# Kernel tuning notes

Measured on AMD Instinct MI355X. Metric: run time of the kernel, lower is better.

The kernel has to match this reference:

```python
import jax, jax.numpy as jnp
import numpy as np
from jax import lax

B = 8192          # batched independent VAD frames (original module is batch=1 streaming)
CUTOFF = 129      # STFT_CUTOFF
STRIDE = 128      # STFT_STRIDE
NFFT = 256        # STFT kernel length (inferred: pad 576->640, stride 128 -> 4 frames)
H = 128           # LSTM hidden size


def conv1d(x, w, b=None, stride=1, padding=0):
    # x: [B, Cin, T], w: [Cout, Cin, K]
    y = lax.conv_general_dilated(x, w, (stride,), [(padding, padding)],
                                 dimension_numbers=("NCH", "OIH", "NCH"))
    if b is not None:
        y = y + b[None, :, None]
    return y


def setup_inputs() -> dict:
    key = jax.random.key(0)
    ks = jax.random.split(key, 40)
    f32 = jnp.float32

    def rn(i, shape, scale=0.1):
        return jax.random.normal(ks[i], shape, dtype=f32) * scale

    inp = {
        "audio": jax.random.normal(ks[0], (B, 576), dtype=f32),
        "h": jnp.zeros((B, H), dtype=f32),
        "c": jnp.zeros((B, H), dtype=f32),
        # STFT basis: 129 real + 129 imag cosine/sine rows, kernel 256
        "forward_basis": rn(1, (2 * CUTOFF, 1, NFFT), 0.1),
        # encoder: 4 conv1d+relu blocks (Silero v5 layout)
        "enc_w1": rn(2, (128, 129, 3)), "enc_b1": rn(3, (128,)),
        "enc_w2": rn(4, (64, 128, 3)), "enc_b2": rn(5, (64,)),
        "enc_w3": rn(6, (64, 64, 3)),  "enc_b3": rn(7, (64,)),
        "enc_w4": rn(8, (128, 64, 3)), "enc_b4": rn(9, (128,)),
        # LSTM cell weights
        "wi": rn(10, (H, H)), "wf": rn(11, (H, H)), "wg": rn(12, (H, H)), "wo": rn(13, (H, H)),
        "ui": rn(14, (H, H)), "uf": rn(15, (H, H)), "ug": rn(16, (H, H)), "uo": rn(17, (H, H)),
        "bxi": rn(18, (H,)), "bxf": rn(19, (H,)), "bxg": rn(20, (H,)), "bxo": rn(21, (H,)),
        "bhi": rn(22, (H,)), "bhf": rn(23, (H,)), "bhg": rn(24, (H,)), "bho": rn(25, (H,)),
        # output head: conv1d 128 -> 1, kernel 1
        "conv_w": rn(26, (1, H, 1)), "conv_b": rn(27, (1,)),
    }
    return inp


def reference(audio, h, c, forward_basis,
              enc_w1, enc_b1, enc_w2, enc_b2, enc_w3, enc_b3, enc_w4, enc_b4,
              wi, wf, wg, wo, ui, uf, ug, uo,
              bxi, bxf, bxg, bxo, bhi, bhf, bhg, bho,
              conv_w, conv_b):
    # STFT via strided conv1d on reflect-padded audio
    x = jnp.pad(audio, ((0, 0), (0, 64)), mode="reflect")[:, None, :]   # [B,1,640]
    x = conv1d(x, forward_basis, stride=STRIDE)                          # [B,258,4]
    real, imag = x[:, :CUTOFF, :], x[:, CUTOFF:, :]
    mag = jnp.sqrt(real ** 2 + imag ** 2)                                # [B,129,4]

    # encoder: conv+relu stack, T: 4 -> 4 -> 2 -> 1 -> 1
    e = jax.nn.relu(conv1d(mag, enc_w1, enc_b1, stride=1, padding=1))
    e = jax.nn.relu(conv1d(e, enc_w2, enc_b2, stride=2, padding=1))
    e = jax.nn.relu(conv1d(e, enc_w3, enc_b3, stride=2, padding=1))
    e = jax.nn.relu(conv1d(e, enc_w4, enc_b4, stride=1, padding=1))
    x = e[:, :, 0]                                                       # [B,128]

    lin = lambda v, W, b: v @ W.T + b
    i_gate = jax.nn.sigmoid(lin(x, wi, bxi) + lin(h, ui, bhi))
    f_gate = jax.nn.sigmoid(lin(x, wf, bxf) + lin(h, uf, bhf))
    g_gate = jnp.tanh(lin(x, wg, bxg) + lin(h, ug, bhg))
    o_gate = jax.nn.sigmoid(lin(x, wo, bxo) + lin(h, uo, bho))
    c_out = f_gate * c + i_gate * g_gate
    h_out = o_gate * jnp.tanh(c_out)

    # output head: relu -> conv1d(128->1, k=1) -> sigmoid -> mean over T(=1)
    y = jax.nn.relu(h_out)                                               # [B,128]
    logit = y @ conv_w[0, :, 0] + conv_b[0]                              # [B]
    prob = jax.nn.sigmoid(logit)[:, None]                                # [B,1]
    return prob, h_out, c_out
```

## Files before the change

### kernel.cpp

```cpp
#include <hip/hip_runtime.h>
#include <math.h>

#define BATCH 8192
typedef unsigned short u16;
typedef unsigned int u32;
typedef _Float16 f16;
typedef __attribute__((ext_vector_type(8))) _Float16 f16x8;
typedef __attribute__((ext_vector_type(4))) float f32x4;
typedef __attribute__((ext_vector_type(4))) unsigned short u16x4;

__device__ __forceinline__ float sigm(float v) { return 1.0f / (1.0f + __expf(-v)); }
__device__ __forceinline__ u16 f2h(float f) {
    union { f16 h; u16 u; } v; v.h = (f16)f;
    return v.u;
}
__device__ __forceinline__ f16x8 ffrag(const u16* Bf, int nt, int ch, int nch, int lane) {
    return *(const f16x8*)(Bf + (((size_t)nt * nch + ch) * 64 + lane) * 8);
}
#define MFMA16(a, b, c) __builtin_amdgcn_mfma_f32_16x16x32_f16(a, b, c, 0, 0, 0)

#define S_FBT 69632
#define S_B1  61440
#define S_B2A 16384
#define S_B2B 24576
#define S_B3  8192
#define S_B4  8192
#define S_BL  131072
#define P_FBT 0
#define P_B1  69632
#define P_B2A 131072
#define P_B2B 147456
#define P_B3  172032
#define P_B4  180224
#define P_BL  188416
#define N_PREP 319488

__global__ __launch_bounds__(256) void k_prep(const float* __restrict__ fb,
                                              const float* __restrict__ w1, const float* __restrict__ w2,
                                              const float* __restrict__ w3, const float* __restrict__ w4,
                                              const float* __restrict__ wi, const float* __restrict__ wf,
                                              const float* __restrict__ wg, const float* __restrict__ wo,
                                              const float* __restrict__ ui, const float* __restrict__ uf,
                                              const float* __restrict__ ug, const float* __restrict__ uo,
                                              u16* __restrict__ wsu) {
    const float* Ws[8] = {wi, wf, wg, wo, ui, uf, ug, uo};
    for (int i = blockIdx.x * 256 + threadIdx.x; i < N_PREP; i += gridDim.x * 256) {
        int r = i;
        float v; int P, idx;
        if (r < S_FBT) {
            int f = r >> 9, lane = (r & 511) >> 3, e = r & 7;
            int n = (f >> 3) * 16 + (lane & 15), k = (f & 7) * 32 + (lane >> 4) * 8 + e;
            int c = n >> 1, part = n & 1;
            v = (n < 258) ? fb[(size_t)(c + part * 129) * 256 + k] : 0.f;
            P = P_FBT; idx = r;
        } else if ((r -= S_FBT) < S_B1) {
            int kk = r / 20480, r2 = r - kk * 20480;
            int f = r2 >> 9, lane = (r2 & 511) >> 3, e = r2 & 7;
            int n = (f / 5) * 16 + (lane & 15), k = (f % 5) * 32 + (lane >> 4) * 8 + e;
            v = (k < 129) ? w1[(size_t)n * 387 + k * 3 + kk] : 0.f;
            P = P_B1; idx = r;
        } else if ((r -= S_B1) < S_B2A) {
            int f = r >> 9, lane = (r & 511) >> 3, e = r & 7;
            int n = (f >> 3) * 16 + (lane & 15), k = (f & 7) * 32 + (lane >> 4) * 8 + e;
            v = w2[(size_t)n * 384 + (k & 127) * 3 + (k >> 7) + 1];
            P = P_B2A; idx = r;
        } else if ((r -= S_B2A) < S_B2B) {
            int f = r >> 9, lane = (r & 511) >> 3, e = r & 7;
            int n = (f / 12) * 16 + (lane & 15), k = (f % 12) * 32 + (lane >> 4) * 8 + e;
            v = w2[(size_t)n * 384 + (k & 127) * 3 + (k >> 7)];
            P = P_B2B; idx = r;
        } else if ((r -= S_B2B) < S_B3) {
            int f = r >> 9, lane = (r & 511) >> 3, e = r & 7;
            int n = (f >> 2) * 16 + (lane & 15), k = (f & 3) * 32 + (lane >> 4) * 8 + e;
            v = w3[(size_t)n * 192 + (k & 63) * 3 + (k >> 6) + 1];
            P = P_B3; idx = r;
        } else if ((r -= S_B3) < S_B4) {
            int f = r >> 9, lane = (r & 511) >> 3, e = r & 7;
            int n = (f >> 1) * 16 + (lane & 15), k = (f & 1) * 32 + (lane >> 4) * 8 + e;
            v = w4[(size_t)n * 192 + k * 3 + 1];
            P = P_B4; idx = r;
        } else {
            r -= S_B4;
            int f = r >> 9, lane = (r & 511) >> 3, e = r & 7;
            int n = (f >> 3) * 16 + (lane & 15), k = (f & 7) * 32 + (lane >> 4) * 8 + e;
            int g = n >> 7, j = n & 127;
            v = Ws[g + ((k >= 128) ? 4 : 0)][(size_t)j * 128 + (k & 127)];
            P = P_BL; idx = r;
        }
        wsu[P + idx] = f2h(v);
    }
}

__global__ __launch_bounds__(512, 4) void k_all(const float* __restrict__ audio,
                                             const u16* __restrict__ wsu,
                                             const float* __restrict__ hin, const float* __restrict__ cin,
                                             const float* __restrict__ b1, const float* __restrict__ b2,
                                             const float* __restrict__ b3, const float* __restrict__ b4,
                                             const float* __restrict__ bxi, const float* __restrict__ bxf,
                                             const float* __restrict__ bxg, const float* __restrict__ bxo,
                                             const float* __restrict__ bhi, const float* __restrict__ bhf,
                                             const float* __restrict__ bhg, const float* __restrict__ bho,
                                             const float* __restrict__ cw, const float* __restrict__ cb,
                                             float* __restrict__ out) {
    __shared__ __align__(16) u16 uni[31872];
    u16* aA = uni;
    u16* eA = uni;
    u16* mA = uni + 11520;
    u16* s2 = uni + 11520;
    u16* s3 = uni + 13696;
    float* pr = (float*)(uni + 14848);
    u16* xh = uni + 27648;
    const int tid = threadIdx.x;
    const int b0 = blockIdx.x << 4;
    for (int i = tid; i < 16 * 160; i += 512) {
        int bb = i / 160, j4 = (i - bb * 160) * 4;
        const float* ap = audio + (size_t)(b0 + bb) * 576;
        float4 v;
        if (j4 < 576) v = *(const float4*)(ap + j4);
        else { v.x = ap[1150 - j4]; v.y = ap[1149 - j4]; v.z = ap[1148 - j4]; v.w = ap[1147 - j4]; }
        int phys = bb * 720 + j4 + (j4 >> 7) * 8;
        u16x4 hv = {f2h(v.x), f2h(v.y), f2h(v.z), f2h(v.w)};
        *(u16x4*)(aA + phys) = hv;
    }
    for (int i = tid; i < 8064; i += 512) ((u32*)mA)[i] = 0u;
    for (int i = tid; i < 16 * 32; i += 512) {
        int row = i >> 5, c4 = (i & 31) * 4;
        float4 v = *(const float4*)(hin + (size_t)(b0 + row) * 128 + c4);
        u16x4 hv = {f2h(v.x), f2h(v.y), f2h(v.z), f2h(v.w)};
        *(u16x4*)(xh + row * 264 + 128 + c4) = hv;
    }
    __syncthreads();
    const int lane = tid & 63, w = tid >> 6;
    const int m = lane & 15, quad = lane >> 4;
    const u16* fbT = wsu + P_FBT;
    const int tcnt = (w == 7) ? 3 : 2;
    f32x4 acc[4][3];
    #pragma unroll
    for (int mt = 0; mt < 4; ++mt)
        #pragma unroll
        for (int t = 0; t < 3; ++t) acc[mt][t] = (f32x4){0.f, 0.f, 0.f, 0.f};
    for (int ch = 0; ch < 8; ++ch) {
        f16x8 ah[4];
        #pragma unroll
        for (int mt = 0; mt < 4; ++mt) {
            int Rm = mt * 16 + m;
            int phys = (Rm >> 2) * 720 + (Rm & 3) * 136 + ch * 32 + quad * 8 + ((ch >= 4) ? 8 : 0);
            ah[mt] = *(const f16x8*)(aA + phys);
        }
        #pragma unroll
        for (int tt = 0; tt < 3; ++tt) {
            if (tt < tcnt) {
                int t = w * 2 + tt;
                f16x8 bh = ffrag(fbT, t, ch, 8, lane);
                #pragma unroll
                for (int mt = 0; mt < 4; ++mt)
                    acc[mt][tt] = MFMA16(ah[mt], bh, acc[mt][tt]);
            }
        }
    }
    #pragma unroll
    for (int tt = 0; tt < 3; ++tt) {
        if (tt < tcnt) {
            int n = (w * 2 + tt) * 16 + m;
            #pragma unroll
            for (int mt = 0; mt < 4; ++mt)
                #pragma unroll
                for (int r = 0; r < 4; ++r) {
                    float vv = acc[mt][tt][r];
                    float s = vv * vv;
                    s += __shfl_xor(s, 1);
                    if (!(n & 1)) {
                        int R = mt * 16 + quad * 4 + r;
                        int bb = R >> 2, t = R & 3, c = n >> 1;
                        mA[(bb * 6 + t + 1) * 168 + c] = f2h(sqrtf(s));
                    }
                }
        }
    }
    __syncthreads();
    const u16* B1p = wsu + P_B1;
    f32x4 acc2[4];
    #pragma unroll
    for (int mt = 0; mt < 4; ++mt) acc2[mt] = (f32x4){0.f, 0.f, 0.f, 0.f};
    for (int kk = 0; kk < 3; ++kk) {
        for (int ch = 0; ch < 5; ++ch) {
            f16x8 bh = ffrag(B1p + kk * 20480, w, ch, 5, lane);
            #pragma unroll
            for (int mt = 0; mt < 4; ++mt) {
                int Rm = mt * 16 + m;
                int phys = ((Rm >> 2) * 6 + (Rm & 3) + kk) * 168 + ch * 32 + quad * 8;
                f16x8 ah = *(const f16x8*)(mA + phys);
                acc2[mt] = MFMA16(ah, bh, acc2[mt]);
            }
        }
    }
    {
        int n = w * 16 + m;
        float bv = b1[n];
        #pragma unroll
        for (int mt = 0; mt < 4; ++mt)
            #pragma unroll
            for (int r = 0; r < 4; ++r) {
                int R = mt * 16 + quad * 4 + r;
                float vv = fmaxf(acc2[mt][r] + bv, 0.f);
                eA[(R >> 2) * 520 + (R & 3) * 128 + n] = f2h(vv);
            }
    }
    __syncthreads();
    {
        const int isB = w >> 2, nt = w & 3;
        const int awoff = isB ? 128 : 0;
        const int nch = isB ? 12 : 8;
        const u16* Bp = wsu + (isB ? P_B2B : P_B2A);
        f32x4 a2 = (f32x4){0.f, 0.f, 0.f, 0.f};
        for (int ch = 0; ch < nch; ++ch) {
            int phys = m * 520 + awoff + ch * 32 + quad * 8;
            f16x8 ah = *(const f16x8*)(eA + phys);
            f16x8 bh = ffrag(Bp, nt, ch, nch, lane);
            a2 = MFMA16(ah, bh, a2);
        }
        const int oc = nt * 16 + m;
        const float bv = b2[oc];
        const int col = isB * 64 + oc;
        #pragma unroll
        for (int r = 0; r < 4; ++r) {
            int row = quad * 4 + r;
            float vv = fmaxf(a2[r] + bv, 0.f);
            s2[row * 136 + col] = f2h(vv);
        }
    }
    __syncthreads();
    if (w < 4) {
        const u16* Bp = wsu + P_B3;
        f32x4 a3 = (f32x4){0.f, 0.f, 0.f, 0.f};
        for (int ch = 0; ch < 4; ++ch) {
            int phys = m * 136 + ch * 32 + quad * 8;
            f16x8 ah = *(const f16x8*)(s2 + phys);
            f16x8 bh = ffrag(Bp, w, ch, 4, lane);
            a3 = MFMA16(ah, bh, a3);
        }
        const int n = w * 16 + m;
        const float bv = b3[n];
        #pragma unroll
        for (int r = 0; r < 4; ++r) {
            int row = quad * 4 + r;
            float vv = fmaxf(a3[r] + bv, 0.f);
            s3[row * 72 + n] = f2h(vv);
        }
    }
    __syncthreads();
    {
        const u16* Bp = wsu + P_B4;
        f32x4 a4 = (f32x4){0.f, 0.f, 0.f, 0.f};
        for (int ch = 0; ch < 2; ++ch) {
            int phys = m * 72 + ch * 32 + quad * 8;
            f16x8 ah = *(const f16x8*)(s3 + phys);
            f16x8 bh = ffrag(Bp, w, ch, 2, lane);
            a4 = MFMA16(ah, bh, a4);
        }
        const int n = w * 16 + m;
        const float bv = b4[n];
        #pragma unroll
        for (int r = 0; r < 4; ++r) {
            int row = quad * 4 + r;
            float vv = fmaxf(a4[r] + bv, 0.f);
            xh[row * 264 + n] = f2h(vv);
        }
    }
    __syncthreads();
    {
        const u16* BLp = wsu + P_BL;
        f32x4 ag[4];
        #pragma unroll
        for (int g = 0; g < 4; ++g) ag[g] = (f32x4){0.f, 0.f, 0.f, 0.f};
        #pragma unroll 2
        for (int ch = 0; ch < 8; ++ch) {
            int phys = m * 264 + ch * 32 + quad * 8;
            f16x8 ah = *(const f16x8*)(xh + phys);
            #pragma unroll
            for (int g = 0; g < 4; ++g) {
                int nt = g * 8 + w;
                f16x8 bh = ffrag(BLp, nt, ch, 8, lane);
                ag[g] = MFMA16(ah, bh, ag[g]);
            }
        }
        float partial[4];
        const int j = w * 16 + m;
        const float bi = bxi[j] + bhi[j];
        const float bff = bxf[j] + bhf[j];
        const float bgg = bxg[j] + bhg[j];
        const float boo = bxo[j] + bho[j];
        const float cwj = cw[j];
        #pragma unroll
        for (int r = 0; r < 4; ++r) {
            const int b = b0 + quad * 4 + r;
            const float ig = sigm(ag[0][r] + bi);
            const float fg = sigm(ag[1][r] + bff);
            const float gg = tanhf(ag[2][r] + bgg);
            const float og = sigm(ag[3][r] + boo);
            const float ci = cin[(size_t)b * 128 + j];
            const float co = fg * ci + ig * gg;
            const float ho = og * tanhf(co);
            out[(size_t)BATCH + (size_t)b * 128 + j] = ho;
            out[(size_t)BATCH + (size_t)BATCH * 128 + (size_t)b * 128 + j] = co;
            partial[r] = fmaxf(ho, 0.f) * cwj;
        }
        #pragma unroll
        for (int off = 1; off < 16; off <<= 1)
            #pragma unroll
            for (int r = 0; r < 4; ++r) partial[r] += __shfl_xor(partial[r], off);
        if (m == 0) {
            #pragma unroll
            for (int r = 0; r < 4; ++r) pr[w * 16 + quad * 4 + r] = partial[r];
        }
    }
    __syncthreads();
    if (tid < 16) {
        float s = cb[0];
        #pragma unroll
        for (int g = 0; g < 8; ++g) s += pr[g * 16 + tid];
        out[b0 + tid] = sigm(s);
    }
}

extern "C" void kernel_launch(void* const* d_in, const int* in_sizes, int n_in,
                              void* d_out, int out_size, void* d_ws, size_t ws_size,
                              hipStream_t stream) {
    const float* audio = (const float*)d_in[0];
    const float* hin   = (const float*)d_in[1];
    const float* cin   = (const float*)d_in[2];
    const float* fb    = (const float*)d_in[3];
    const float* w1    = (const float*)d_in[4];
    const float* b1    = (const float*)d_in[5];
    const float* w2    = (const float*)d_in[6];
    const float* b2    = (const float*)d_in[7];
    const float* w3    = (const float*)d_in[8];
    const float* b3    = (const float*)d_in[9];
    const float* w4    = (const float*)d_in[10];
    const float* b4    = (const float*)d_in[11];
    const float* wi    = (const float*)d_in[12];
    const float* wf    = (const float*)d_in[13];
    const float* wg    = (const float*)d_in[14];
    const float* wo    = (const float*)d_in[15];
    const float* ui    = (const float*)d_in[16];
    const float* uf    = (const float*)d_in[17];
    const float* ug    = (const float*)d_in[18];
    const float* uo    = (const float*)d_in[19];
    const float* bxi   = (const float*)d_in[20];
    const float* bxf   = (const float*)d_in[21];
    const float* bxg   = (const float*)d_in[22];
    const float* bxo   = (const float*)d_in[23];
    const float* bhi   = (const float*)d_in[24];
    const float* bhf   = (const float*)d_in[25];
    const float* bhg   = (const float*)d_in[26];
    const float* bho   = (const float*)d_in[27];
    const float* cw    = (const float*)d_in[28];
    const float* cb    = (const float*)d_in[29];
    float* out = (float*)d_out;

    u16* wsu = (u16*)d_ws;

    k_prep<<<640, 256, 0, stream>>>(fb, w1, w2, w3, w4, wi, wf, wg, wo, ui, uf, ug, uo, wsu);
    k_all<<<BATCH / 16, 512, 0, stream>>>(audio, wsu, hin, cin, b1, b2, b3, b4,
                                          bxi, bxf, bxg, bxo, bhi, bhf, bhg, bho,
                                          cw, cb, out);
}
```

Baseline: 158.9 us.

## Prefetch weight fragments before barriers and split MFMA accumulators into two chains

Each encoder and LSTM stage now loads its B-operand weight fragments from global memory into registers before the preceding __syncthreads, so those loads overlap with the barrier wait and the previous stage's tail. The K loops are fully unrolled and alternate between two independent accumulators, which shortens the dependent MFMA chains. The cost is higher register pressure: 15 fragments are held for B1 and 12 for B2, which may lower occupancy.

```diff
diff --git a/kernel.cpp b/kernel.cpp
--- a/kernel.cpp
+++ b/kernel.cpp
@@ -177,14 +177,22 @@
                 }
         }
     }
-    __syncthreads();
     const u16* B1p = wsu + P_B1;
+    f16x8 pB1[15];
+    #pragma unroll
+    for (int kk = 0; kk < 3; ++kk)
+        #pragma unroll
+        for (int ch = 0; ch < 5; ++ch)
+            pB1[kk * 5 + ch] = ffrag(B1p + kk * 20480, w, ch, 5, lane);
+    __syncthreads();
     f32x4 acc2[4];
     #pragma unroll
     for (int mt = 0; mt < 4; ++mt) acc2[mt] = (f32x4){0.f, 0.f, 0.f, 0.f};
+    #pragma unroll
     for (int kk = 0; kk < 3; ++kk) {
+        #pragma unroll
         for (int ch = 0; ch < 5; ++ch) {
-            f16x8 bh = ffrag(B1p + kk * 20480, w, ch, 5, lane);
+            f16x8 bh = pB1[kk * 5 + ch];
             #pragma unroll
             for (int mt = 0; mt < 4; ++mt) {
                 int Rm = mt * 16 + m;
@@ -206,82 +214,118 @@
                 eA[(R >> 2) * 520 + (R & 3) * 128 + n] = f2h(vv);
             }
     }
+    const int isB = w >> 2, nt2 = w & 3;
+    const int nch2 = isB ? 12 : 8;
+    const u16* Bp2 = wsu + (isB ? P_B2B : P_B2A);
+    f16x8 pB2[12];
+    #pragma unroll
+    for (int ch = 0; ch < 8; ++ch) pB2[ch] = ffrag(Bp2, nt2, ch, nch2, lane);
+    if (isB) {
+        #pragma unroll
+        for (int ch = 8; ch < 12; ++ch) pB2[ch] = ffrag(Bp2, nt2, ch, 12, lane);
+    }
     __syncthreads();
     {
-        const int isB = w >> 2, nt = w & 3;
         const int awoff = isB ? 128 : 0;
-        const int nch = isB ? 12 : 8;
-        const u16* Bp = wsu + (isB ? P_B2B : P_B2A);
-        f32x4 a2 = (f32x4){0.f, 0.f, 0.f, 0.f};
-        for (int ch = 0; ch < nch; ++ch) {
+        f32x4 a2a = (f32x4){0.f, 0.f, 0.f, 0.f};
+        f32x4 a2b = (f32x4){0.f, 0.f, 0.f, 0.f};
+        #pragma unroll
+        for (int ch = 0; ch < 8; ++ch) {
             int phys = m * 520 + awoff + ch * 32 + quad * 8;
             f16x8 ah = *(const f16x8*)(eA + phys);
-            f16x8 bh = ffrag(Bp, nt, ch, nch, lane);
-            a2 = MFMA16(ah, bh, a2);
-        }
-        const int oc = nt * 16 + m;
+            if (ch & 1) a2b = MFMA16(ah, pB2[ch], a2b);
+            else        a2a = MFMA16(ah, pB2[ch], a2a);
+        }
+        if (isB) {
+            #pragma unroll
+            for (int ch = 8; ch < 12; ++ch) {
+                int phys = m * 520 + awoff + ch * 32 + quad * 8;
+                f16x8 ah = *(const f16x8*)(eA + phys);
+                if (ch & 1) a2b = MFMA16(ah, pB2[ch], a2b);
+                else        a2a = MFMA16(ah, pB2[ch], a2a);
+            }
+        }
+        const int oc = nt2 * 16 + m;
         const float bv = b2[oc];
         const int col = isB * 64 + oc;
         #pragma unroll
         for (int r = 0; r < 4; ++r) {
             int row = quad * 4 + r;
-            float vv = fmaxf(a2[r] + bv, 0.f);
+            float vv = fmaxf(a2a[r] + a2b[r] + bv, 0.f);
             s2[row * 136 + col] = f2h(vv);
         }
     }
-    __syncthreads();
+    f16x8 pB3[4];
     if (w < 4) {
-        const u16* Bp = wsu + P_B3;
-        f32x4 a3 = (f32x4){0.f, 0.f, 0.f, 0.f};
+        #pragma unroll
+        for (int ch = 0; ch < 4; ++ch) pB3[ch] = ffrag(wsu + P_B3, w, ch, 4, lane);
+    }
+    __syncthreads();
+    if (w < 4) {
+        f32x4 a3a = (f32x4){0.f, 0.f, 0.f, 0.f};
+        f32x4 a3b = (f32x4){0.f, 0.f, 0.f, 0.f};
+        #pragma unroll
         for (int ch = 0; ch < 4; ++ch) {
             int phys = m * 136 + ch * 32 + quad * 8;
             f16x8 ah = *(const f16x8*)(s2 + phys);
-            f16x8 bh = ffrag(Bp, w, ch, 4, lane);
-            a3 = MFMA16(ah, bh, a3);
+            if (ch & 1) a3b = MFMA16(ah, pB3[ch], a3b);
+            else        a3a = MFMA16(ah, pB3[ch], a3a);
         }
         const int n = w * 16 + m;
         const float bv = b3[n];
         #pragma unroll
         for (int r = 0; r < 4; ++r) {
             int row = quad * 4 + r;
-            float vv = fmaxf(a3[r] + bv, 0.f);
+            float vv = fmaxf(a3a[r] + a3b[r] + bv, 0.f);
             s3[row * 72 + n] = f2h(vv);
         }
     }
+    f16x8 pB4[2];
+    #pragma unroll
+    for (int ch = 0; ch < 2; ++ch) pB4[ch] = ffrag(wsu + P_B4, w, ch, 2, lane);
     __syncthreads();
     {
-        const u16* Bp = wsu + P_B4;
-        f32x4 a4 = (f32x4){0.f, 0.f, 0.f, 0.f};
-        for (int ch = 0; ch < 2; ++ch) {
-            int phys = m * 72 + ch * 32 + quad * 8;
-            f16x8 ah = *(const f16x8*)(s3 + phys);
-            f16x8 bh = ffrag(Bp, w, ch, 2, lane);
-            a4 = MFMA16(ah, bh, a4);
+        f32x4 a4a = (f32x4){0.f, 0.f, 0.f, 0.f};
+        f32x4 a4b = (f32x4){0.f, 0.f, 0.f, 0.f};
+        {
+            int phys = m * 72 + 0 * 32 + quad * 8;
+            a4a = MFMA16(*(const f16x8*)(s3 + phys), pB4[0], a4a);
+            phys = m * 72 + 1 * 32 + quad * 8;
+            a4b = MFMA16(*(const f16x8*)(s3 + phys), pB4[1], a4b);
         }
         const int n = w * 16 + m;
         const float bv = b4[n];
         #pragma unroll
         for (int r = 0; r < 4; ++r) {
             int row = quad * 4 + r;
-            float vv = fmaxf(a4[r] + bv, 0.f);
+            float vv = fmaxf(a4a[r] + a4b[r] + bv, 0.f);
             xh[row * 264 + n] = f2h(vv);
         }
     }
+    const u16* BLp = wsu + P_BL;
+    f16x8 pBL[8];
+    #pragma unroll
+    for (int ch = 0; ch < 2; ++ch)
+        #pragma unroll
+        for (int g = 0; g < 4; ++g)
+            pBL[g * 2 + ch] = ffrag(BLp, g * 8 + w, ch, 8, lane);
     __syncthreads();
     {
-        const u16* BLp = wsu + P_BL;
-        f32x4 ag[4];
-        #pragma unroll
-        for (int g = 0; g < 4; ++g) ag[g] = (f32x4){0.f, 0.f, 0.f, 0.f};
-        #pragma unroll 2
+        f32x4 agA[4], agB[4];
+        #pragma unroll
+        for (int g = 0; g < 4; ++g) {
+            agA[g] = (f32x4){0.f, 0.f, 0.f, 0.f};
+            agB[g] = (f32x4){0.f, 0.f, 0.f, 0.f};
+        }
+        #pragma unroll
         for (int ch = 0; ch < 8; ++ch) {
             int phys = m * 264 + ch * 32 + quad * 8;
             f16x8 ah = *(const f16x8*)(xh + phys);
             #pragma unroll
             for (int g = 0; g < 4; ++g) {
-                int nt = g * 8 + w;
-                f16x8 bh = ffrag(BLp, nt, ch, 8, lane);
-                ag[g] = MFMA16(ah, bh, ag[g]);
+                f16x8 bh = (ch < 2) ? pBL[g * 2 + ch] : ffrag(BLp, g * 8 + w, ch, 8, lane);
+                if (ch & 1) agB[g] = MFMA16(ah, bh, agB[g]);
+                else        agA[g] = MFMA16(ah, bh, agA[g]);
             }
         }
         float partial[4];
@@ -294,10 +338,10 @@
         #pragma unroll
         for (int r = 0; r < 4; ++r) {
             const int b = b0 + quad * 4 + r;
-            const float ig = sigm(ag[0][r] + bi);
-            const float fg = sigm(ag[1][r] + bff);
-            const float gg = tanhf(ag[2][r] + bgg);
-            const float og = sigm(ag[3][r] + boo);
+            const float ig = sigm(agA[0][r] + agB[0][r] + bi);
+            const float fg = sigm(agA[1][r] + agB[1][r] + bff);
+            const float gg = tanhf(agA[2][r] + agB[2][r] + bgg);
+            const float og = sigm(agA[3][r] + agB[3][r] + boo);
             const float ci = cin[(size_t)b * 128 + j];
             const float co = fg * ci + ig * gg;
             const float ho = og * tanhf(co);
```

Result: faster. 155.7 us (-2.1%).
